# Kernel tuning notes

Hardware: AMD Instinct MI355X
Metric: run time of the kernel (lower is better)

Reference implementation:

```python
import jax, jax.numpy as jnp
import numpy as np

D_MODEL = 1024
N_HEADS = 16
D_K = D_MODEL // N_HEADS
THETA = 10000.0
B, S = 4, 2048


def _rope(x, positions):
    # x: [B, H, S, D_K]; positions: [S] int
    half = D_K // 2
    inv_freq = THETA ** (-jnp.arange(0, half, dtype=jnp.float32) * 2.0 / D_K)  # [half]
    ang = positions.astype(jnp.float32)[:, None] * inv_freq[None, :]  # [S, half]
    cos = jnp.cos(ang)[None, None, :, :]
    sin = jnp.sin(ang)[None, None, :, :]
    x_even = x[..., 0::2]
    x_odd = x[..., 1::2]
    out_even = x_even * cos - x_odd * sin
    out_odd = x_even * sin + x_odd * cos
    # interleave back to original layout
    out = jnp.stack([out_even, out_odd], axis=-1).reshape(x.shape)
    return out


def setup_inputs() -> dict:
    key = jax.random.key(0)
    ks = jax.random.split(key, 5)
    scale = 1.0 / np.sqrt(D_MODEL)
    return {
        "x": jax.random.normal(ks[0], (B, S, D_MODEL), dtype=jnp.float32),
        "token_positions": jnp.arange(S, dtype=jnp.int64 if jax.config.jax_enable_x64 else jnp.int32),
        "Wq": jax.random.normal(ks[1], (D_MODEL, D_MODEL), dtype=jnp.float32) * scale,
        "Wk": jax.random.normal(ks[2], (D_MODEL, D_MODEL), dtype=jnp.float32) * scale,
        "Wv": jax.random.normal(ks[3], (D_MODEL, D_MODEL), dtype=jnp.float32) * scale,
        "Wo": jax.random.normal(ks[4], (D_MODEL, D_MODEL), dtype=jnp.float32) * scale,
    }


def reference(x, token_positions, Wq, Wk, Wv, Wo):
    bsz, seq_len, _ = x.shape
    # projections (Linear_Transform: y = x @ W^T, no bias)
    def proj(W):
        h = jnp.einsum("bsd,ed->bse", x, W)
        return h.reshape(bsz, seq_len, N_HEADS, D_K).transpose(0, 2, 1, 3)  # [B,H,S,Dk]
    Q = proj(Wq)
    K = proj(Wk)
    V = proj(Wv)
    Q = _rope(Q, token_positions)
    K = _rope(K, token_positions)
    # scaled dot product attention with causal mask
    scores = jnp.einsum("bhqd,bhkd->bhqk", Q, K) / jnp.sqrt(jnp.float32(D_K))
    causal = jnp.tril(jnp.ones((seq_len, seq_len), dtype=bool))  # [S,S]
    scores = jnp.where(causal[None, None, :, :], scores, -jnp.inf)
    attn = jax.nn.softmax(scores, axis=-1)
    out = jnp.einsum("bhqk,bhkd->bhqd", attn, V)
    out = out.transpose(0, 2, 1, 3).reshape(bsz, seq_len, D_MODEL)
    return jnp.einsum("bsd,ed->bse", out, Wo)
```

## Files before the change

kernel.cpp:

```cpp
#include <hip/hip_runtime.h>
#include <hip/hip_bf16.h>
#include <cstdint>
#include <cstddef>

typedef __attribute__((ext_vector_type(4))) float f32x4;
typedef __attribute__((ext_vector_type(16))) float f32x16;
typedef __attribute__((ext_vector_type(8))) short bf16x8;
typedef unsigned int u32;
typedef unsigned short u16;


__device__ __forceinline__ u16 f2bf(float x) {
  u32 u = __builtin_bit_cast(u32, x);
  u += 0x7fffu + ((u >> 16) & 1u);
  return (u16)(u >> 16);
}

__device__ __forceinline__ u32 cvt_pk_bf16(float lo, float hi) {
  u32 r;
  asm("v_cvt_pk_bf16_f32 %0, %1, %2" : "=v"(r) : "v"(lo), "v"(hi));
  return r;
}

__device__ __forceinline__ float fexp2(float x) {
  float r;
  asm("v_exp_f32 %0, %1\n\ts_nop 1" : "=v"(r) : "v"(x));
  return r;
}

__device__ __forceinline__ void perm_swap(u32& a, u32& b) {
  asm("v_permlane32_swap_b32 %0, %1" : "+v"(a), "+v"(b));
}

__device__ __forceinline__ void gl_lds16(const void* g, void* l) {
  __builtin_amdgcn_global_load_lds(
      (const __attribute__((address_space(1))) u32*)(uintptr_t)g,
      (__attribute__((address_space(3))) u32*)(u32)(uintptr_t)l,
      16, 0, 0);
}

#define MFMA16(a, b, c) __builtin_amdgcn_mfma_f32_16x16x32_bf16((a), (b), (c), 0, 0, 0)
#define MFMA32(a, b, c) __builtin_amdgcn_mfma_f32_32x32x16_bf16((a), (b), (c), 0, 0, 0)
#define SBAR() do { __builtin_amdgcn_sched_barrier(0); __builtin_amdgcn_s_barrier(); \
                    __builtin_amdgcn_sched_barrier(0); } while (0)
#define SCHED_FENCE() __builtin_amdgcn_sched_barrier(0)


__global__ void cast_all_k(const float* __restrict__ x, const float* __restrict__ wq,
                           const float* __restrict__ wk, const float* __restrict__ wv,
                           const float* __restrict__ wo, u16* __restrict__ xb,
                           u16* __restrict__ wqb, u16* __restrict__ wkb,
                           u16* __restrict__ wvb, u16* __restrict__ wob) {
  int blk = blockIdx.x;
  const float* s; u16* d; int i;
  if (blk < 8192)       { s = x;  d = xb;  i = blk * 256; }
  else if (blk < 9216)  { s = wq; d = wqb; i = (blk - 8192) * 256; }
  else if (blk < 10240) { s = wk; d = wkb; i = (blk - 9216) * 256; }
  else if (blk < 11264) { s = wv; d = wvb; i = (blk - 10240) * 256; }
  else                  { s = wo; d = wob; i = (blk - 11264) * 256; }
  i += threadIdx.x;
  const float4 v = reinterpret_cast<const float4*>(s)[i];
  uint2 o;
  o.x = cvt_pk_bf16(v.x, v.y);
  o.y = cvt_pk_bf16(v.z, v.w);
  reinterpret_cast<uint2*>(d)[i] = o;
}


__global__ void rope_table_k(const int* __restrict__ pos, float2* __restrict__ cs) {
  int idx = blockIdx.x * 256 + threadIdx.x;
  int s = idx >> 5, i = idx & 31;
  float inv = powf(10000.0f, -(float)i * (1.0f / 32.0f));
  float ang = (float)pos[s] * inv;
  cs[idx] = float2{cosf(ang), sinf(ang)};
}


__global__ __launch_bounds__(512)
void gemm_qkv(const u16* __restrict__ A, const u16* __restrict__ B,
              const float2* __restrict__ cs, u16* __restrict__ Qr,
              u16* __restrict__ Kr, u16* __restrict__ Vt, float qscale) {
  const int K = 1024;
  __shared__ u16 a_lds[2][256 * 64];
  __shared__ u16 b_lds[2][256 * 64];

  const int tid = threadIdx.x, l = tid & 63;
  const int wid = tid >> 6;
  const int wr = wid >> 2, wc = wid & 3;
  const int c = l & 15, h4 = l >> 4;

  const int id = blockIdx.x;
  const int k48 = id >> 3, xcd = id & 7;
  const int bm = xcd * 4 + k48 / 12, bn = k48 % 12;

  const u16* Ab = A + (size_t)bm * 256 * K;
  const u16* Bb = B + (size_t)bn * 256 * K;

  auto stageA = [&](int s, int chunk, int k0) {
    int t5 = chunk * 512 + tid;
    int row = t5 >> 3, slot = t5 & 7;
    int sp = slot ^ (row & 7);
    gl_lds16(Ab + (size_t)row * K + k0 + sp * 8, &a_lds[s][t5 * 8]);
  };
  auto stageB = [&](int s, int chunk, int k0) {
    int t5 = chunk * 512 + tid;
    int row = t5 >> 3, slot = t5 & 7;
    int sp = slot ^ (row & 7);
    gl_lds16(Bb + (size_t)row * K + k0 + sp * 8, &b_lds[s][t5 * 8]);
  };

  const f32x4 fz = {0.f, 0.f, 0.f, 0.f};
  f32x4 acc[8][4];
#pragma unroll
  for (int mi = 0; mi < 8; ++mi)
#pragma unroll
    for (int ni = 0; ni < 4; ++ni) acc[mi][ni] = fz;

#pragma unroll
  for (int ch = 0; ch < 4; ++ch) stageA(0, ch, 0);
#pragma unroll
  for (int ch = 0; ch < 4; ++ch) stageB(0, ch, 0);
  asm volatile("s_waitcnt vmcnt(0)" ::: "memory");
  SBAR();

  const int nk = K >> 6;
#pragma unroll 1
  for (int t = 0; t < nk; ++t) {
    const int s = t & 1;
    const int k1 = (t + 1) << 6;
    const bool st = (t + 1 < nk);

    bf16x8 bfr[4][2];
#pragma unroll
    for (int ni = 0; ni < 4; ++ni)
#pragma unroll
      for (int kk = 0; kk < 2; ++kk) {
        int row = wc * 64 + ni * 16 + c;
        int sp = (kk * 4 + h4) ^ (row & 7);
        bfr[ni][kk] = *(const bf16x8*)&b_lds[s][row * 64 + sp * 8];
      }

#pragma unroll
    for (int p = 0; p < 4; ++p) {
      bf16x8 af[2][2];
#pragma unroll
      for (int m2 = 0; m2 < 2; ++m2)
#pragma unroll
        for (int kk = 0; kk < 2; ++kk) {
          int mi = p * 2 + m2;
          int row = wr * 128 + mi * 16 + c;
          int sp = (kk * 4 + h4) ^ (row & 7);
          af[m2][kk] = *(const bf16x8*)&a_lds[s][row * 64 + sp * 8];
        }
      if (st) {
        if (p < 2) { stageA(s ^ 1, p * 2, k1); stageA(s ^ 1, p * 2 + 1, k1); }
        else       { stageB(s ^ 1, (p - 2) * 2, k1); stageB(s ^ 1, (p - 2) * 2 + 1, k1); }
      }
      SCHED_FENCE();
      __builtin_amdgcn_s_setprio(1);
#pragma unroll
      for (int m2 = 0; m2 < 2; ++m2)
#pragma unroll
        for (int ni = 0; ni < 4; ++ni)
#pragma unroll
          for (int kk = 0; kk < 2; ++kk)
            acc[p * 2 + m2][ni] = MFMA16(af[m2][kk], bfr[ni][kk], acc[p * 2 + m2][ni]);
      __builtin_amdgcn_s_setprio(0);
      SCHED_FENCE();
    }

    asm volatile("s_waitcnt vmcnt(0)" ::: "memory");
    SBAR();
  }

  const int sector = bn >> 2;
  const int colb = ((bn & 3) << 8) + wc * 64;

  if (sector == 2) {
#pragma unroll
    for (int mi = 0; mi < 8; ++mi) {
      int row = bm * 256 + wr * 128 + mi * 16 + 4 * h4;
      int b_ = row >> 11, s = row & 2047;
#pragma unroll
      for (int ni = 0; ni < 4; ++ni) {
        int cv = colb + ni * 16 + c;
        int hh = cv >> 6, dk = cv & 63;
        f32x4 v = acc[mi][ni];
        uint2 st;
        st.x = cvt_pk_bf16(v[0], v[1]);
        st.y = cvt_pk_bf16(v[2], v[3]);
        *(uint2*)&Vt[(((size_t)b_ * 16 + hh) << 17) + ((size_t)dk << 11) + s] = st;
      }
    }
  } else {
    u16* dst = sector ? Kr : Qr;
    const float scale = sector ? 1.0f : qscale;
#pragma unroll
    for (int mi = 0; mi < 8; ++mi) {
      int row0 = bm * 256 + wr * 128 + mi * 16 + 4 * h4;
#pragma unroll
      for (int ni = 0; ni < 4; ++ni) {
        int cv = colb + ni * 16 + c;
        int hh = cv >> 6, i2 = cv & 63;
        f32x4 v = acc[mi][ni];
        f32x4 pv;
#pragma unroll
        for (int j = 0; j < 4; ++j) pv[j] = __shfl_xor(v[j], 1);
        if (!(l & 1)) {
#pragma unroll
          for (int j = 0; j < 4; ++j) {
            int r = row0 + j, s = r & 2047, b_ = r >> 11;
            float2 tt = cs[(s << 5) + (i2 >> 1)];
            float oe = (v[j] * tt.x - pv[j] * tt.y) * scale;
            float oo = (v[j] * tt.y + pv[j] * tt.x) * scale;
            *(u32*)&dst[(((size_t)(b_ * 16 + hh) * 2048 + s) << 6) + i2] =
                cvt_pk_bf16(oe, oo);
          }
        }
      }
    }
  }
}


__global__ __launch_bounds__(256, 3)
void gemm_bt(const u16* __restrict__ A, const u16* __restrict__ B,
             float* __restrict__ C, int M, int N, int K) {
  __shared__ u16 a_lds[3][128 * 32];
  __shared__ u16 b_lds[3][128 * 32];
  const int tid = threadIdx.x;
  const int l = tid & 63;
  const int w = tid >> 6;
  const int wm = w >> 1, wn = w & 1;
  const int bm = blockIdx.y, bn = blockIdx.x;
  const int c = l & 15, h4 = l >> 4;

  const u16* Ab = A + (size_t)bm * 128 * K;
  const u16* Bb = B + (size_t)bn * 128 * K;

  auto stage = [&](int sl, int k0) {
#pragma unroll
    for (int half = 0; half < 2; ++half) {
      int t = half * 256 + tid;
      int row = t >> 2, slot = t & 3;
      int sp = slot ^ ((row >> 1) & 3);
      gl_lds16(Ab + (size_t)row * K + k0 + sp * 8, &a_lds[sl][t * 8]);
      gl_lds16(Bb + (size_t)row * K + k0 + sp * 8, &b_lds[sl][t * 8]);
    }
  };

  const f32x4 fz = {0.f, 0.f, 0.f, 0.f};
  f32x4 acc[4][4];
#pragma unroll
  for (int mi = 0; mi < 4; ++mi)
#pragma unroll
    for (int ni = 0; ni < 4; ++ni) acc[mi][ni] = fz;

  const int nk = K >> 5;
  stage(0, 0);
  stage(1, 32);

  int sl = 0;
#pragma unroll 1
  for (int t = 0; t < nk; ++t) {
    if (t + 2 < nk) {
      int s2 = sl + 2; if (s2 >= 3) s2 -= 3;
      stage(s2, (t + 2) * 32);
      __builtin_amdgcn_sched_barrier(0);
      asm volatile("s_waitcnt vmcnt(8)" ::: "memory");
    } else if (t + 1 < nk) {
      asm volatile("s_waitcnt vmcnt(4)" ::: "memory");
    } else {
      asm volatile("s_waitcnt vmcnt(0)" ::: "memory");
    }
    SBAR();

    bf16x8 af[4], bf[4];
#pragma unroll
    for (int mi = 0; mi < 4; ++mi) {
      int row = wm * 64 + mi * 16 + c;
      int sp = h4 ^ ((row >> 1) & 3);
      af[mi] = *(const bf16x8*)&a_lds[sl][row * 32 + sp * 8];
    }
#pragma unroll
    for (int ni = 0; ni < 4; ++ni) {
      int row = wn * 64 + ni * 16 + c;
      int sp = h4 ^ ((row >> 1) & 3);
      bf[ni] = *(const bf16x8*)&b_lds[sl][row * 32 + sp * 8];
    }
    __builtin_amdgcn_s_setprio(1);
#pragma unroll
    for (int mi = 0; mi < 4; ++mi)
#pragma unroll
      for (int ni = 0; ni < 4; ++ni)
        acc[mi][ni] = MFMA16(af[mi], bf[ni], acc[mi][ni]);
    __builtin_amdgcn_s_setprio(0);

    sl = (sl == 2) ? 0 : sl + 1;
  }

#pragma unroll
  for (int mi = 0; mi < 4; ++mi) {
    int rbase = bm * 128 + wm * 64 + mi * 16 + ((l >> 4) << 2);
#pragma unroll
    for (int ni = 0; ni < 4; ++ni) {
      int col = bn * 128 + wn * 64 + ni * 16 + (l & 15);
      f32x4 v = acc[mi][ni];
#pragma unroll
      for (int j = 0; j < 4; ++j)
        C[(size_t)(rbase + j) * N + col] = v[j];
    }
  }
}


__global__ __launch_bounds__(256, 2)
void attn_k(const u16* __restrict__ Q, const u16* __restrict__ K,
            const u16* __restrict__ V, u16* __restrict__ O) {
  const int S = 2048;
  __shared__ u16 k_lds[3][64 * 64];
  __shared__ u16 v_lds[3][64 * 64];

  const int tid = threadIdx.x, l = tid & 63, w = tid >> 6;
  const int lane31 = l & 31, hi = l >> 5;

  const int wg = blockIdx.x;
  const int idx = (wg & 7) * 64 + (wg >> 3);
  const int bh = idx >> 3, pairI = idx & 7;

  const u16* Kb = K + (size_t)bh * S * 64;
  const u16* Vb = V + (size_t)bh * 64 * S;
  const int b = bh >> 4, hd = bh & 15;

  auto stageKV = [&](int bq, int kv0) {
#pragma unroll
    for (int half = 0; half < 2; ++half) {
      int t = half * 256 + tid;
      int row = t >> 3, slot = t & 7;
      int sp = slot ^ (row & 7);
      gl_lds16(Kb + (size_t)(kv0 + row) * 64 + sp * 8, &k_lds[bq][t * 8]);
      gl_lds16(Vb + (size_t)row * S + kv0 + sp * 8, &v_lds[bq][t * 8]);
    }
  };

#pragma unroll 1
  for (int ph = 0; ph < 2; ++ph) {
    const int qi = ph ? (15 - pairI) : pairI;
    const int q0 = qi * 128;
    const int nkv = 2 * qi + 2;
    const int qrow = q0 + w * 32 + lane31;
    const u16* Qp = Q + ((size_t)bh * S + qrow) * 64;

    bf16x8 qf[4];
#pragma unroll
    for (int ks = 0; ks < 4; ++ks)
      qf[ks] = *(const bf16x8*)(Qp + ks * 16 + hi * 8);
    __builtin_amdgcn_sched_barrier(0);
    stageKV(0, 0);
    stageKV(1, 64);

    f32x16 oacc[2];
#pragma unroll
    for (int dt = 0; dt < 2; ++dt)
#pragma unroll
      for (int r = 0; r < 16; ++r) oacc[dt][r] = 0.f;
    float m_run = -1e30f, l_run = 0.f;

    int buf = 0;
#pragma unroll 1
    for (int t = 0; t < nkv; ++t) {
      if (t + 2 < nkv) {
        int b2 = buf + 2; if (b2 >= 3) b2 -= 3;
        stageKV(b2, (t + 2) * 64);
        __builtin_amdgcn_sched_barrier(0);
        asm volatile("s_waitcnt vmcnt(8)" ::: "memory");
      } else if (t + 1 < nkv) {
        asm volatile("s_waitcnt vmcnt(4)" ::: "memory");
      } else {
        asm volatile("s_waitcnt vmcnt(0)" ::: "memory");
      }
      SBAR();

      f32x16 sc[2];
#pragma unroll
      for (int dt = 0; dt < 2; ++dt)
#pragma unroll
        for (int r = 0; r < 16; ++r) sc[dt][r] = 0.f;
      __builtin_amdgcn_s_setprio(1);
#pragma unroll
      for (int ks = 0; ks < 4; ++ks) {
        int sp = (2 * ks + hi) ^ (lane31 & 7);
#pragma unroll
        for (int dt = 0; dt < 2; ++dt) {
          bf16x8 kf = *(const bf16x8*)&k_lds[buf][(dt * 32 + lane31) * 64 + sp * 8];
          sc[dt] = MFMA32(kf, qf[ks], sc[dt]);
        }
      }
      __builtin_amdgcn_s_setprio(0);

      bf16x8 vf[2][4];
#pragma unroll
      for (int ks = 0; ks < 4; ++ks) {
        int sp = (2 * ks + hi) ^ (lane31 & 7);
#pragma unroll
        for (int dt = 0; dt < 2; ++dt)
          vf[dt][ks] = *(const bf16x8*)&v_lds[buf][(dt * 32 + lane31) * 64 + sp * 8];
      }

      if (t >= nkv - 2) {
#pragma unroll
        for (int dt = 0; dt < 2; ++dt)
#pragma unroll
          for (int r = 0; r < 16; ++r) {
            int kvg = t * 64 + dt * 32 + (r & 3) + 8 * (r >> 2) + 4 * hi;
            if (kvg > qrow) sc[dt][r] = -1e30f;
          }
      }

      float r16[16];
#pragma unroll
      for (int i = 0; i < 16; ++i) r16[i] = fmaxf(sc[0][i], sc[1][i]);
#pragma unroll
      for (int i = 0; i < 8; ++i) r16[i] = fmaxf(r16[i], r16[i + 8]);
#pragma unroll
      for (int i = 0; i < 4; ++i) r16[i] = fmaxf(r16[i], r16[i + 4]);
      float mx = fmaxf(fmaxf(r16[0], r16[1]), fmaxf(r16[2], r16[3]));
      mx = fmaxf(mx, __shfl_xor(mx, 32));

      const bool nores = __all(mx <= m_run);
      float mnew = nores ? m_run : fmaxf(m_run, mx);
#pragma unroll
      for (int dt = 0; dt < 2; ++dt)
#pragma unroll
        for (int r = 0; r < 16; ++r) sc[dt][r] = fexp2(sc[dt][r] - mnew);
      float s16[16];
#pragma unroll
      for (int i = 0; i < 16; ++i) s16[i] = sc[0][i] + sc[1][i];
#pragma unroll
      for (int i = 0; i < 8; ++i) s16[i] += s16[i + 8];
#pragma unroll
      for (int i = 0; i < 4; ++i) s16[i] += s16[i + 4];
      float ps = (s16[0] + s16[1]) + (s16[2] + s16[3]);
      ps += __shfl_xor(ps, 32);

      if (nores) {
        l_run += ps;
      } else {
        float alpha = fexp2(m_run - mnew);
        l_run = l_run * alpha + ps;
        m_run = mnew;
#pragma unroll
        for (int dt = 0; dt < 2; ++dt)
#pragma unroll
          for (int r = 0; r < 16; ++r) oacc[dt][r] *= alpha;
      }

      union { u32 u[4]; bf16x8 v; } pf[4];
#pragma unroll
      for (int ks = 0; ks < 4; ++ks) {
        const int sidx = ks >> 1, rb = (ks & 1) * 8;
        u32 c01 = cvt_pk_bf16(sc[sidx][rb + 0], sc[sidx][rb + 1]);
        u32 c23 = cvt_pk_bf16(sc[sidx][rb + 2], sc[sidx][rb + 3]);
        u32 c45 = cvt_pk_bf16(sc[sidx][rb + 4], sc[sidx][rb + 5]);
        u32 c67 = cvt_pk_bf16(sc[sidx][rb + 6], sc[sidx][rb + 7]);
        perm_swap(c01, c45);
        perm_swap(c23, c67);
        pf[ks].u[0] = c01; pf[ks].u[1] = c23; pf[ks].u[2] = c45; pf[ks].u[3] = c67;
      }

      __builtin_amdgcn_s_setprio(1);
#pragma unroll
      for (int dt = 0; dt < 2; ++dt)
#pragma unroll
        for (int ks = 0; ks < 4; ++ks)
          oacc[dt] = MFMA32(vf[dt][ks], pf[ks].v, oacc[dt]);
      __builtin_amdgcn_s_setprio(0);

      buf = (buf == 2) ? 0 : buf + 1;
    }

    SBAR();

    float inv = 1.f / l_run;
    u16* Ob = O + (((size_t)(b * 2048 + qrow)) << 10) + hd * 64;
#pragma unroll
    for (int dt = 0; dt < 2; ++dt)
#pragma unroll
      for (int g = 0; g < 4; ++g) {
        uint2 st;
        st.x = cvt_pk_bf16(oacc[dt][4 * g + 0] * inv, oacc[dt][4 * g + 1] * inv);
        st.y = cvt_pk_bf16(oacc[dt][4 * g + 2] * inv, oacc[dt][4 * g + 3] * inv);
        *(uint2*)&Ob[dt * 32 + g * 8 + hi * 4] = st;
      }
  }
}


extern "C" void kernel_launch(void* const* d_in, const int* in_sizes, int n_in,
                              void* d_out, int out_size, void* d_ws, size_t ws_size,
                              hipStream_t stream) {
  (void)in_sizes; (void)n_in; (void)out_size; (void)ws_size;
  const float* x  = (const float*)d_in[0];
  const int* pos  = (const int*)d_in[1];
  const float* Wq = (const float*)d_in[2];
  const float* Wk = (const float*)d_in[3];
  const float* Wv = (const float*)d_in[4];
  const float* Wo = (const float*)d_in[5];
  float* out = (float*)d_out;

  const int S = 2048, D = 1024;
  const size_t M = (size_t)4 * S;

  char* ws = (char*)d_ws;
  size_t off = 0;
  auto alloc = [&](size_t bytes) {
    void* p = ws + off;
    off += (bytes + 255) & ~(size_t)255;
    return p;
  };
  u16* xb   = (u16*)alloc(M * D * 2);
  u16* wqb  = (u16*)alloc((size_t)D * D * 2);
  u16* wkb  = (u16*)alloc((size_t)D * D * 2);
  u16* wvb  = (u16*)alloc((size_t)D * D * 2);
  u16* wob  = (u16*)alloc((size_t)D * D * 2);
  u16* Qr   = (u16*)alloc(M * D * 2);
  u16* Kr   = (u16*)alloc(M * D * 2);
  u16* Vt   = (u16*)alloc(M * D * 2);
  u16* Ob   = (u16*)alloc(M * D * 2);
  float2* csT = (float2*)alloc((size_t)S * 32 * 8);

  cast_all_k<<<12288, 256, 0, stream>>>(x, Wq, Wk, Wv, Wo, xb, wqb, wkb, wvb, wob);
  rope_table_k<<<(S * 32) / 256, 256, 0, stream>>>(pos, csT);

  const float QSCALE = 0.125f * 1.4426950408889634f;

  gemm_qkv<<<384, 512, 0, stream>>>(xb, wqb, csT, Qr, Kr, Vt, QSCALE);
  attn_k<<<512, 256, 0, stream>>>(Qr, Kr, Vt, Ob);
  gemm_bt<<<dim3(8, (unsigned)(M / 128)), 256, 0, stream>>>(Ob, wob, out, (int)M, D, D);
}
```

Before: 183.5 us.

## Shrink attention workgroups to 64-query tiles with double-buffered KV staging

```diff
diff --git a/kernel.cpp b/kernel.cpp
--- a/kernel.cpp
+++ b/kernel.cpp
@@ -314,19 +314,19 @@
 }
 
 
-__global__ __launch_bounds__(256, 2)
+__global__ __launch_bounds__(128)
 void attn_k(const u16* __restrict__ Q, const u16* __restrict__ K,
             const u16* __restrict__ V, u16* __restrict__ O) {
   const int S = 2048;
-  __shared__ u16 k_lds[3][64 * 64];
-  __shared__ u16 v_lds[3][64 * 64];
+  __shared__ u16 k_lds[2][64 * 64];
+  __shared__ u16 v_lds[2][64 * 64];
 
   const int tid = threadIdx.x, l = tid & 63, w = tid >> 6;
   const int lane31 = l & 31, hi = l >> 5;
 
   const int wg = blockIdx.x;
-  const int idx = (wg & 7) * 64 + (wg >> 3);
-  const int bh = idx >> 3, pairI = idx & 7;
+  const int idx = (wg & 7) * 128 + (wg >> 3);
+  const int bh = idx >> 4, pairI = idx & 15;
 
   const u16* Kb = K + (size_t)bh * S * 64;
   const u16* Vb = V + (size_t)bh * 64 * S;
@@ -334,20 +334,20 @@
 
   auto stageKV = [&](int bq, int kv0) {
 #pragma unroll
-    for (int half = 0; half < 2; ++half) {
-      int t = half * 256 + tid;
-      int row = t >> 3, slot = t & 7;
+    for (int ch = 0; ch < 4; ++ch) {
+      int t5 = ch * 128 + tid;
+      int row = t5 >> 3, slot = t5 & 7;
       int sp = slot ^ (row & 7);
-      gl_lds16(Kb + (size_t)(kv0 + row) * 64 + sp * 8, &k_lds[bq][t * 8]);
-      gl_lds16(Vb + (size_t)row * S + kv0 + sp * 8, &v_lds[bq][t * 8]);
+      gl_lds16(Kb + (size_t)(kv0 + row) * 64 + sp * 8, &k_lds[bq][t5 * 8]);
+      gl_lds16(Vb + (size_t)row * S + kv0 + sp * 8, &v_lds[bq][t5 * 8]);
     }
   };
 
 #pragma unroll 1
   for (int ph = 0; ph < 2; ++ph) {
-    const int qi = ph ? (15 - pairI) : pairI;
-    const int q0 = qi * 128;
-    const int nkv = 2 * qi + 2;
+    const int g = ph ? (31 - pairI) : pairI;
+    const int q0 = g * 64;
+    const int nt = g + 1;
     const int qrow = q0 + w * 32 + lane31;
     const u16* Qp = Q + ((size_t)bh * S + qrow) * 64;
 
@@ -357,7 +357,6 @@
       qf[ks] = *(const bf16x8*)(Qp + ks * 16 + hi * 8);
     __builtin_amdgcn_sched_barrier(0);
     stageKV(0, 0);
-    stageKV(1, 64);
 
     f32x16 oacc[2];
 #pragma unroll
@@ -366,20 +365,13 @@
       for (int r = 0; r < 16; ++r) oacc[dt][r] = 0.f;
     float m_run = -1e30f, l_run = 0.f;
 
-    int buf = 0;
+    int slot = 0;
 #pragma unroll 1
-    for (int t = 0; t < nkv; ++t) {
-      if (t + 2 < nkv) {
-        int b2 = buf + 2; if (b2 >= 3) b2 -= 3;
-        stageKV(b2, (t + 2) * 64);
-        __builtin_amdgcn_sched_barrier(0);
-        asm volatile("s_waitcnt vmcnt(8)" ::: "memory");
-      } else if (t + 1 < nkv) {
-        asm volatile("s_waitcnt vmcnt(4)" ::: "memory");
-      } else {
-        asm volatile("s_waitcnt vmcnt(0)" ::: "memory");
-      }
+    for (int t = 0; t < nt; ++t) {
+      asm volatile("s_waitcnt vmcnt(0)" ::: "memory");
       SBAR();
+      if (t + 1 < nt) stageKV(slot ^ 1, (t + 1) * 64);
+      __builtin_amdgcn_sched_barrier(0);
 
       f32x16 sc[2];
 #pragma unroll
@@ -392,7 +384,7 @@
         int sp = (2 * ks + hi) ^ (lane31 & 7);
 #pragma unroll
         for (int dt = 0; dt < 2; ++dt) {
-          bf16x8 kf = *(const bf16x8*)&k_lds[buf][(dt * 32 + lane31) * 64 + sp * 8];
+          bf16x8 kf = *(const bf16x8*)&k_lds[slot][(dt * 32 + lane31) * 64 + sp * 8];
           sc[dt] = MFMA32(kf, qf[ks], sc[dt]);
         }
       }
@@ -404,10 +396,10 @@
         int sp = (2 * ks + hi) ^ (lane31 & 7);
 #pragma unroll
         for (int dt = 0; dt < 2; ++dt)
-          vf[dt][ks] = *(const bf16x8*)&v_lds[buf][(dt * 32 + lane31) * 64 + sp * 8];
-      }
-
-      if (t >= nkv - 2) {
+          vf[dt][ks] = *(const bf16x8*)&v_lds[slot][(dt * 32 + lane31) * 64 + sp * 8];
+      }
+
+      if (t == nt - 1) {
 #pragma unroll
         for (int dt = 0; dt < 2; ++dt)
 #pragma unroll
@@ -476,7 +468,7 @@
           oacc[dt] = MFMA32(vf[dt][ks], pf[ks].v, oacc[dt]);
       __builtin_amdgcn_s_setprio(0);
 
-      buf = (buf == 2) ? 0 : buf + 1;
+      slot ^= 1;
     }
 
     SBAR();
@@ -486,11 +478,11 @@
 #pragma unroll
     for (int dt = 0; dt < 2; ++dt)
 #pragma unroll
-      for (int g = 0; g < 4; ++g) {
+      for (int g2 = 0; g2 < 4; ++g2) {
         uint2 st;
-        st.x = cvt_pk_bf16(oacc[dt][4 * g + 0] * inv, oacc[dt][4 * g + 1] * inv);
-        st.y = cvt_pk_bf16(oacc[dt][4 * g + 2] * inv, oacc[dt][4 * g + 3] * inv);
-        *(uint2*)&Ob[dt * 32 + g * 8 + hi * 4] = st;
+        st.x = cvt_pk_bf16(oacc[dt][4 * g2 + 0] * inv, oacc[dt][4 * g2 + 1] * inv);
+        st.y = cvt_pk_bf16(oacc[dt][4 * g2 + 2] * inv, oacc[dt][4 * g2 + 3] * inv);
+        *(uint2*)&Ob[dt * 32 + g2 * 8 + hi * 4] = st;
       }
   }
 }
@@ -535,6 +527,6 @@
   const float QSCALE = 0.125f * 1.4426950408889634f;
 
   gemm_qkv<<<384, 512, 0, stream>>>(xb, wqb, csT, Qr, Kr, Vt, QSCALE);
-  attn_k<<<512, 256, 0, stream>>>(Qr, Kr, Vt, Ob);
+  attn_k<<<1024, 128, 0, stream>>>(Qr, Kr, Vt, Ob);
   gemm_bt<<<dim3(8, (unsigned)(M / 128)), 256, 0, stream>>>(Ob, wob, out, (int)M, D, D);
 }
```

After: 216.3 us. 1.18x slower.
